# Optimization experiments

Hardware: AMD Instinct MI355X
Metric: run time of the kernel (lower is better)

## Reference

```python
import jax, jax.numpy as jnp
import numpy as np

N, F, H = 100000, 128, 2
DH = F // H  # per-head dim = 64
E = 1600000


def setup_inputs() -> dict:
    key = jax.random.key(0)
    ks = jax.random.split(key, 10)
    s = 0.05
    return {
        "nodes": jax.random.normal(ks[0], (N, F), jnp.float32),
        "edge_index": jax.random.randint(ks[1], (2, E), 0, N, jnp.int64),
        # TransformerConv linear layers (stored as [in, out] so we do x @ W)
        "Wq": jax.random.normal(ks[2], (F, F), jnp.float32) * s,
        "bq": jnp.zeros((F,), jnp.float32),
        "Wk": jax.random.normal(ks[3], (F, F), jnp.float32) * s,
        "bk": jnp.zeros((F,), jnp.float32),
        "Wv": jax.random.normal(ks[4], (F, F), jnp.float32) * s,
        "bv": jnp.zeros((F,), jnp.float32),
        "Wskip": jax.random.normal(ks[5], (F, F), jnp.float32) * s,
        "bskip": jnp.zeros((F,), jnp.float32),
        # gate: Linear(2F, F, bias=False); fuse: Linear(F, F, bias=False)
        "Wgate": jax.random.normal(ks[6], (2 * F, F), jnp.float32) * s,
        "Wfuse": jax.random.normal(ks[7], (F, F), jnp.float32) * s,
    }


def transformer_conv(nodes, src, dst, Wq, bq, Wk, bk, Wv, bv, Wskip, bskip):
    n = nodes.shape[0]
    q = (nodes @ Wq + bq).reshape(n, H, DH)
    k = (nodes @ Wk + bk).reshape(n, H, DH)
    v = (nodes @ Wv + bv).reshape(n, H, DH)
    # per-edge attention logits: [E, H]
    alpha = jnp.einsum("ehd,ehd->eh", q[dst], k[src]) / jnp.sqrt(jnp.float32(DH))
    # segment softmax over incoming edges of each destination node
    amax = jax.ops.segment_max(alpha, dst, num_segments=n)  # [N, H]
    ex = jnp.exp(alpha - amax[dst])
    denom = jax.ops.segment_sum(ex, dst, num_segments=n)  # [N, H]
    w = ex / denom[dst]  # [E, H]
    msg = v[src] * w[:, :, None]  # [E, H, DH]
    agg = jax.ops.segment_sum(msg, dst, num_segments=n).reshape(n, F)
    # root/skip connection (beta=0 -> plain add)
    return agg + nodes @ Wskip + bskip


def reference(nodes, edge_index, Wq, bq, Wk, bk, Wv, bv, Wskip, bskip, Wgate, Wfuse):
    src, dst = edge_index[0], edge_index[1]
    x = transformer_conv(nodes, src, dst, Wq, bq, Wk, bk, Wv, bv, Wskip, bskip)
    h = jnp.concatenate([nodes, x], axis=-1)  # [N, 2F]
    gate = jax.nn.sigmoid(h @ Wgate)  # [N, F]
    fuse = jnp.tanh(x @ Wfuse)  # [N, F]
    return gate * fuse + (1.0 - gate) * nodes
```

## Files before the change

kernel.cpp:

```cpp
#include <hip/hip_runtime.h>
#include <hip/hip_fp8.h>
#include <stdint.h>

#define NN 100000
#define EE 1600000
#define FF 128
#define CAP 60

typedef __attribute__((ext_vector_type(8)))  short bf16x8;
typedef __attribute__((ext_vector_type(8)))  unsigned short u16x8;
typedef __attribute__((ext_vector_type(2)))  float f32x2;
typedef __attribute__((ext_vector_type(16))) float f32x16;

#define NB_BLOCKS    6250
#define PREP_BLOCKS  450
#define CNT0_BLOCKS  98
#define BUILD2_BLOCKS 1563
#define QKVS_BLOCKS  12500
#define F2_BLOCKS    (BUILD2_BLOCKS + QKVS_BLOCKS)

__device__ __forceinline__ float bf2f(unsigned short u) {
    union { unsigned int i; float f; } c; c.i = ((unsigned int)u) << 16; return c.f;
}
__device__ __forceinline__ unsigned short f2bf(float f) {
    union { unsigned int i; float f; } c; c.f = f;
    unsigned int u = c.i;
    return (unsigned short)((u + 0x7FFFu + ((u >> 16) & 1u)) >> 16);
}
__device__ __forceinline__ float fp82f(unsigned int b) {
    __hip_fp8_e4m3 t; t.__x = (__hip_fp8_storage_t)(b & 0xFFu); return (float)t;
}
__device__ __forceinline__ unsigned char f2fp8(float f) {
    __hip_fp8_e4m3 t(f); return (unsigned char)t.__x;
}
template<bool HI>
__device__ __forceinline__ f32x2 cvtpk8(unsigned int w) {
#if __has_builtin(__builtin_amdgcn_cvt_pk_f32_fp8)
    return __builtin_amdgcn_cvt_pk_f32_fp8((int)w, HI);
#else
    f32x2 r;
    r[0] = fp82f(HI ? (w >> 16) : w);
    r[1] = fp82f(HI ? (w >> 24) : (w >> 8));
    return r;
#endif
}
__device__ __forceinline__ bf16x8 pack8(const float* p) {
    float4 f0 = *(const float4*)p;
    float4 f1 = *(const float4*)(p + 4);
    bf16x8 r;
    r[0] = (short)f2bf(f0.x); r[1] = (short)f2bf(f0.y);
    r[2] = (short)f2bf(f0.z); r[3] = (short)f2bf(f0.w);
    r[4] = (short)f2bf(f1.x); r[5] = (short)f2bf(f1.y);
    r[6] = (short)f2bf(f1.z); r[7] = (short)f2bf(f1.w);
    return r;
}

__global__ __launch_bounds__(256) void k_f1(
    const float* __restrict__ nodes, unsigned short* __restrict__ nb,
    const float* __restrict__ Wq, const float* __restrict__ Wk,
    const float* __restrict__ Wv, const float* __restrict__ Ws,
    const float* __restrict__ Wg, const float* __restrict__ Wf,
    const float* __restrict__ bq, const float* __restrict__ bk,
    const float* __restrict__ bv, const float* __restrict__ bs,
    unsigned short* __restrict__ Wp, unsigned short* __restrict__ Wp2,
    float* __restrict__ bias, int* __restrict__ count)
{
    const int bid = blockIdx.x;
    if (bid < NB_BLOCKS) {
        size_t i = ((size_t)bid * 256 + threadIdx.x) * 8;
        *(bf16x8*)(nb + i) = pack8(nodes + i);
    } else if (bid < NB_BLOCKS + PREP_BLOCKS) {
        int idx = (bid - NB_BLOCKS) * 256 + threadIdx.x;
        if (idx < 65536) {
            int j = idx & 7, lane = (idx >> 3) & 63, ks = (idx >> 9) & 7;
            int cf = (idx >> 12) & 3, cg = idx >> 14;
            int c  = cf * 32 + (lane & 31);
            int kk = ks * 16 + (lane >> 5) * 8 + j;
            const float* W = (cg == 0) ? Wq : (cg == 1) ? Wk : (cg == 2) ? Wv : Ws;
            Wp[idx] = f2bf(W[kk * FF + c]);
        } else if (idx < 65536 + 49152) {
            int p = idx - 65536;
            int j = p & 7, lane = (p >> 3) & 63, ks = (p >> 9) & 7;
            int cf = (p >> 12) & 3, mat = p >> 14;
            int c  = cf * 32 + (lane & 31);
            int kk = ks * 16 + (lane >> 5) * 8 + j;
            float v = (mat == 0) ? Wg[kk * FF + c]
                    : (mat == 1) ? Wg[(FF + kk) * FF + c]
                                 : Wf[kk * FF + c];
            Wp2[p] = f2bf(v);
        } else if (idx < 65536 + 49152 + 512) {
            int j = idx - (65536 + 49152);
            float b = (j < 128) ? bq[j] : (j < 256) ? bk[j - 128]
                    : (j < 384) ? bv[j - 256] : bs[j - 384];
            bias[j] = b;
        }
    } else {
        int j = ((bid - NB_BLOCKS - PREP_BLOCKS) * 256 + threadIdx.x) * 4;
        if (j < NN) *(int4*)(count + j) = make_int4(0, 0, 0, 0);
    }
}

__global__ __launch_bounds__(256) void k_f2(
    const int* __restrict__ src, const int* __restrict__ dst,
    int* __restrict__ count, int* __restrict__ srclist,
    const unsigned short* __restrict__ nb, const unsigned short* __restrict__ Wp,
    const float* __restrict__ bias, unsigned short* __restrict__ qb,
    unsigned char* __restrict__ kvb, unsigned short* __restrict__ skb)
{
    const int bid = blockIdx.x;
    if (bid % 9 == 0) {
        const int bb = bid / 9;
        const int e0 = bb * 1024 + threadIdx.x;
        #pragma unroll
        for (int j = 0; j < 4; ++j) {
            const int e = e0 + j * 256;
            if (e < EE) {
                int d = dst[e];
                int s = src[e];
                int r = atomicAdd(&count[d], 1);
                if (r < CAP) __builtin_nontemporal_store(s, &srclist[(size_t)d * CAP + r]);
            }
        }
        return;
    }
    const int q = bid - bid / 9 - 1;
    const int row0 = (q >> 2) * 32;
    const int cg = q & 3;
    const int wave = threadIdx.x >> 6, lane = threadIdx.x & 63;
    const int arow = row0 + (lane & 31);
    const int khalf = lane >> 5;
    const int cf = wave;

    f32x16 acc;
    #pragma unroll
    for (int r = 0; r < 16; ++r) acc[r] = 0.f;

    const unsigned short* ap = nb + (size_t)arow * FF + khalf * 8;
    #pragma unroll
    for (int ks = 0; ks < 8; ++ks) {
        bf16x8 a = *(const bf16x8*)(ap + ks * 16);
        bf16x8 b = *(const bf16x8*)(Wp + (((cg * 4 + cf) * 8 + ks) << 9) + (lane << 3));
        acc = __builtin_amdgcn_mfma_f32_32x32x16_bf16(a, b, acc, 0, 0, 0);
    }

    const int col = cf * 32 + (lane & 31);
    const float bv = bias[cg * 128 + col];
    #pragma unroll
    for (int r = 0; r < 16; ++r) {
        const int rr = row0 + (r & 3) + 8 * (r >> 2) + 4 * (lane >> 5);
        const float fv = acc[r] + bv;
        if (cg == 0)      qb [(size_t)rr * 128 + col] = f2bf(fv);
        else if (cg == 1) kvb[(size_t)rr * 256 + (col >> 2) * 8 + (col & 3)]     = f2fp8(fv);
        else if (cg == 2) kvb[(size_t)rr * 256 + (col >> 2) * 8 + 4 + (col & 3)] = f2fp8(fv);
        else              skb[(size_t)rr * 128 + col] = f2bf(fv);
    }
}

__global__ __launch_bounds__(256, 4) void k_f3(
    const unsigned short* __restrict__ nb, const unsigned short* __restrict__ qb,
    const unsigned char* __restrict__ kvb, const unsigned short* __restrict__ skb,
    const unsigned short* __restrict__ Wp2,
    const int* __restrict__ count, const int* __restrict__ srclist,
    float* __restrict__ out)
{
    __shared__ unsigned short xl[32 * 128];
    const int wave = threadIdx.x >> 6, lane = threadIdx.x & 63;
    const int row0 = blockIdx.x * 32;

    const int es = lane >> 4;
    const int le = lane & 15;

    #pragma unroll 1
    for (int i = 0; i < 8; ++i) {
        const int rl  = wave * 8 + i;
        const int wid = row0 + rl;

        const u16x8 qr = *(const u16x8*)(qb + (size_t)wid * FF + le * 8);
        float qa[8];
        #pragma unroll
        for (int j = 0; j < 8; ++j) qa[j] = bf2f(qr[j]) * 0.125f;

        int deg = __builtin_amdgcn_readfirstlane(count[wid]);
        if (deg > CAP) deg = CAP;
        const size_t base = (size_t)wid * CAP;
        const int sreg = srclist[base + (lane < CAP ? lane : CAP - 1)];

        float denom = 0.f;
        float acc[8];
        #pragma unroll
        for (int j = 0; j < 8; ++j) acc[j] = 0.f;

        const int nit = (deg + 3) >> 2;
        #pragma unroll 2
        for (int it = 0; it < nit; ++it) {
            const int idx  = 4 * it + es;
            const int sidx = idx < deg ? idx : deg - 1;
            const int s    = __shfl(sreg, sidx);
            const uint4 kv = *(const uint4*)(kvb + (size_t)s * 256 + le * 16);
            const f32x2 k01 = cvtpk8<false>(kv.x), k23 = cvtpk8<true>(kv.x);
            const f32x2 k45 = cvtpk8<false>(kv.z), k67 = cvtpk8<true>(kv.z);
            float p = qa[0] * k01[0] + qa[1] * k01[1] + qa[2] * k23[0] + qa[3] * k23[1]
                    + qa[4] * k45[0] + qa[5] * k45[1] + qa[6] * k67[0] + qa[7] * k67[1];
            p += __shfl_xor(p, 1);
            p += __shfl_xor(p, 2);
            p += __shfl_xor(p, 4);
            const float ex = (idx < deg) ? __expf(p) : 0.f;
            denom += ex;
            const f32x2 v01 = cvtpk8<false>(kv.y), v23 = cvtpk8<true>(kv.y);
            const f32x2 v45 = cvtpk8<false>(kv.w), v67 = cvtpk8<true>(kv.w);
            acc[0] = fmaf(ex, v01[0], acc[0]); acc[1] = fmaf(ex, v01[1], acc[1]);
            acc[2] = fmaf(ex, v23[0], acc[2]); acc[3] = fmaf(ex, v23[1], acc[3]);
            acc[4] = fmaf(ex, v45[0], acc[4]); acc[5] = fmaf(ex, v45[1], acc[5]);
            acc[6] = fmaf(ex, v67[0], acc[6]); acc[7] = fmaf(ex, v67[1], acc[7]);
        }
        denom += __shfl_xor(denom, 16);
        denom += __shfl_xor(denom, 32);
        #pragma unroll
        for (int j = 0; j < 8; ++j) {
            acc[j] += __shfl_xor(acc[j], 16);
            acc[j] += __shfl_xor(acc[j], 32);
        }

        if (es == 0) {
            const float inv = (denom > 0.f) ? (1.0f / denom) : 0.f;
            const u16x8 sr = *(const u16x8*)(skb + (size_t)wid * FF + le * 8);
            u16x8 o;
            #pragma unroll
            for (int j = 0; j < 8; ++j) o[j] = f2bf(fmaf(acc[j], inv, bf2f(sr[j])));
            *(u16x8*)&xl[rl * 128 + ((le ^ (rl & 7)) << 3)] = o;
        }
    }
    __syncthreads();

    const int arow = row0 + (lane & 31);
    const int khalf = lane >> 5;
    const int cf = wave;

    f32x16 gacc, facc;
    #pragma unroll
    for (int r = 0; r < 16; ++r) { gacc[r] = 0.f; facc[r] = 0.f; }

    #pragma unroll
    for (int ks = 0; ks < 8; ++ks) {
        bf16x8 an = *(const bf16x8*)(nb + (size_t)arow * FF + ks * 16 + khalf * 8);
        const int g2 = ks * 2 + khalf;
        bf16x8 ax = *(const bf16x8*)&xl[(lane & 31) * 128 + ((g2 ^ ((lane & 31) & 7)) << 3)];
        bf16x8 b0 = *(const bf16x8*)(Wp2 + (((0 * 4 + cf) * 8 + ks) << 9) + (lane << 3));
        bf16x8 b1 = *(const bf16x8*)(Wp2 + (((1 * 4 + cf) * 8 + ks) << 9) + (lane << 3));
        bf16x8 b2 = *(const bf16x8*)(Wp2 + (((2 * 4 + cf) * 8 + ks) << 9) + (lane << 3));
        gacc = __builtin_amdgcn_mfma_f32_32x32x16_bf16(an, b0, gacc, 0, 0, 0);
        gacc = __builtin_amdgcn_mfma_f32_32x32x16_bf16(ax, b1, gacc, 0, 0, 0);
        facc = __builtin_amdgcn_mfma_f32_32x32x16_bf16(ax, b2, facc, 0, 0, 0);
    }

    const int col = cf * 32 + (lane & 31);
    #pragma unroll
    for (int r = 0; r < 16; ++r) {
        const int rr = row0 + (r & 3) + 8 * (r >> 2) + 4 * (lane >> 5);
        const float g  = 1.0f / (1.0f + __expf(-gacc[r]));
        const float e2 = __expf(2.0f * facc[r]);
        const float fv = (e2 - 1.0f) / (e2 + 1.0f);
        const float nv = bf2f(nb[(size_t)rr * FF + col]);
        out[(size_t)rr * FF + col] = g * fv + (1.0f - g) * nv;
    }
}

extern "C" void kernel_launch(void* const* d_in, const int* in_sizes, int n_in,
                              void* d_out, int out_size, void* d_ws, size_t ws_size,
                              hipStream_t stream) {
    const float* nodes = (const float*)d_in[0];
    const int*   ei    = (const int*)d_in[1];
    const int*   esrc  = ei;
    const int*   edst  = ei + EE;
    const float* Wq = (const float*)d_in[2];
    const float* bq = (const float*)d_in[3];
    const float* Wk = (const float*)d_in[4];
    const float* bk = (const float*)d_in[5];
    const float* Wv = (const float*)d_in[6];
    const float* bv = (const float*)d_in[7];
    const float* Ws = (const float*)d_in[8];
    const float* bs = (const float*)d_in[9];
    const float* Wg = (const float*)d_in[10];
    const float* Wf = (const float*)d_in[11];
    float* out = (float*)d_out;

    char* wsb = (char*)d_ws;
    unsigned short* qb   = (unsigned short*)wsb;
    unsigned char*  kvb  = (unsigned char*)(qb + (size_t)NN * 128);
    unsigned short* skb  = (unsigned short*)(kvb + (size_t)NN * 256);
    unsigned short* nb   = skb + (size_t)NN * 128;
    unsigned short* Wp   = nb + (size_t)NN * 128;
    unsigned short* Wp2  = Wp + 65536;
    float* bias  = (float*)(Wp2 + 49152);
    int* count   = (int*)(bias + 512);
    int* srclist = count + NN;

    k_f1<<<NB_BLOCKS + PREP_BLOCKS + CNT0_BLOCKS, 256, 0, stream>>>(
        nodes, nb, Wq, Wk, Wv, Ws, Wg, Wf, bq, bk, bv, bs, Wp, Wp2, bias, count);
    k_f2<<<F2_BLOCKS, 256, 0, stream>>>(
        esrc, edst, count, srclist, nb, Wp, bias, qb, kvb, skb);
    k_f3<<<NN / 32, 256, 0, stream>>>(
        nb, qb, kvb, skb, Wp2, count, srclist, out);
}
```

Baseline: 233.7 us.

## Prefetch next row's metadata and use packed math in attention aggregation loop

In the fused aggregation kernel, the per-row loads (degree count, query, source list, skip row) for the next destination row are issued one iteration ahead, so their latency can overlap with the current row's edge loop. The dot product and value accumulation are rewritten with float2 vectors so the compiler can emit packed FMA instructions. The 1/8 query scale is folded together with log2(e) so that exp2f can stand in for __expf. Edge index loads in the CSR build now use nontemporal loads, and the edge loop unroll goes from 2 to 4. These changes add register pressure, which may affect occupancy under the 256,4 launch bounds.

```diff
diff --git a/kernel.cpp b/kernel.cpp
--- a/kernel.cpp
+++ b/kernel.cpp
@@ -18,6 +18,8 @@
 #define BUILD2_BLOCKS 1563
 #define QKVS_BLOCKS  12500
 #define F2_BLOCKS    (BUILD2_BLOCKS + QKVS_BLOCKS)
+
+#define QSCALE 0.1803368801111244f
 
 __device__ __forceinline__ float bf2f(unsigned short u) {
     union { unsigned int i; float f; } c; c.i = ((unsigned int)u) << 16; return c.f;
@@ -115,8 +117,8 @@
         for (int j = 0; j < 4; ++j) {
             const int e = e0 + j * 256;
             if (e < EE) {
-                int d = dst[e];
-                int s = src[e];
+                int d = __builtin_nontemporal_load(&dst[e]);
+                int s = __builtin_nontemporal_load(&src[e]);
                 int r = atomicAdd(&count[d], 1);
                 if (r < CAP) __builtin_nontemporal_store(s, &srclist[(size_t)d * CAP + r]);
             }
@@ -169,64 +171,81 @@
 
     const int es = lane >> 4;
     const int le = lane & 15;
+    const int slane = lane < CAP ? lane : CAP - 1;
+
+    {
+        const int wid0 = row0 + wave * 8;
+    }
+    int   deg_n  = count[row0 + wave * 8];
+    u16x8 qr_n   = *(const u16x8*)(qb  + (size_t)(row0 + wave * 8) * FF + le * 8);
+    int   sreg_n = srclist[(size_t)(row0 + wave * 8) * CAP + slane];
+    u16x8 sr_n   = *(const u16x8*)(skb + (size_t)(row0 + wave * 8) * FF + le * 8);
 
     #pragma unroll 1
     for (int i = 0; i < 8; ++i) {
         const int rl  = wave * 8 + i;
         const int wid = row0 + rl;
 
-        const u16x8 qr = *(const u16x8*)(qb + (size_t)wid * FF + le * 8);
-        float qa[8];
-        #pragma unroll
-        for (int j = 0; j < 8; ++j) qa[j] = bf2f(qr[j]) * 0.125f;
-
-        int deg = __builtin_amdgcn_readfirstlane(count[wid]);
+        int deg = __builtin_amdgcn_readfirstlane(deg_n);
         if (deg > CAP) deg = CAP;
-        const size_t base = (size_t)wid * CAP;
-        const int sreg = srclist[base + (lane < CAP ? lane : CAP - 1)];
+        const u16x8 qr  = qr_n;
+        const int   sreg = sreg_n;
+        const u16x8 sr  = sr_n;
+
+        if (i < 7) {
+            const int widn = wid + 1;
+            deg_n  = count[widn];
+            qr_n   = *(const u16x8*)(qb  + (size_t)widn * FF + le * 8);
+            sreg_n = srclist[(size_t)widn * CAP + slane];
+            sr_n   = *(const u16x8*)(skb + (size_t)widn * FF + le * 8);
+        }
+
+        f32x2 qa0, qa1, qa2, qa3;
+        qa0[0] = bf2f(qr[0]) * QSCALE; qa0[1] = bf2f(qr[1]) * QSCALE;
+        qa1[0] = bf2f(qr[2]) * QSCALE; qa1[1] = bf2f(qr[3]) * QSCALE;
+        qa2[0] = bf2f(qr[4]) * QSCALE; qa2[1] = bf2f(qr[5]) * QSCALE;
+        qa3[0] = bf2f(qr[6]) * QSCALE; qa3[1] = bf2f(qr[7]) * QSCALE;
 
         float denom = 0.f;
-        float acc[8];
-        #pragma unroll
-        for (int j = 0; j < 8; ++j) acc[j] = 0.f;
+        f32x2 a01 = {0.f, 0.f}, a23 = {0.f, 0.f}, a45 = {0.f, 0.f}, a67 = {0.f, 0.f};
 
         const int nit = (deg + 3) >> 2;
-        #pragma unroll 2
+        #pragma unroll 4
         for (int it = 0; it < nit; ++it) {
             const int idx  = 4 * it + es;
             const int sidx = idx < deg ? idx : deg - 1;
             const int s    = __shfl(sreg, sidx);
             const uint4 kv = *(const uint4*)(kvb + (size_t)s * 256 + le * 16);
-            const f32x2 k01 = cvtpk8<false>(kv.x), k23 = cvtpk8<true>(kv.x);
-            const f32x2 k45 = cvtpk8<false>(kv.z), k67 = cvtpk8<true>(kv.z);
-            float p = qa[0] * k01[0] + qa[1] * k01[1] + qa[2] * k23[0] + qa[3] * k23[1]
-                    + qa[4] * k45[0] + qa[5] * k45[1] + qa[6] * k67[0] + qa[7] * k67[1];
+            f32x2 pp = qa0 * cvtpk8<false>(kv.x);
+            pp += qa1 * cvtpk8<true>(kv.x);
+            pp += qa2 * cvtpk8<false>(kv.z);
+            pp += qa3 * cvtpk8<true>(kv.z);
+            float p = pp[0] + pp[1];
             p += __shfl_xor(p, 1);
             p += __shfl_xor(p, 2);
             p += __shfl_xor(p, 4);
-            const float ex = (idx < deg) ? __expf(p) : 0.f;
+            const float ex = (idx < deg) ? exp2f(p) : 0.f;
             denom += ex;
-            const f32x2 v01 = cvtpk8<false>(kv.y), v23 = cvtpk8<true>(kv.y);
-            const f32x2 v45 = cvtpk8<false>(kv.w), v67 = cvtpk8<true>(kv.w);
-            acc[0] = fmaf(ex, v01[0], acc[0]); acc[1] = fmaf(ex, v01[1], acc[1]);
-            acc[2] = fmaf(ex, v23[0], acc[2]); acc[3] = fmaf(ex, v23[1], acc[3]);
-            acc[4] = fmaf(ex, v45[0], acc[4]); acc[5] = fmaf(ex, v45[1], acc[5]);
-            acc[6] = fmaf(ex, v67[0], acc[6]); acc[7] = fmaf(ex, v67[1], acc[7]);
+            f32x2 exv; exv[0] = ex; exv[1] = ex;
+            a01 += exv * cvtpk8<false>(kv.y);
+            a23 += exv * cvtpk8<true>(kv.y);
+            a45 += exv * cvtpk8<false>(kv.w);
+            a67 += exv * cvtpk8<true>(kv.w);
         }
         denom += __shfl_xor(denom, 16);
         denom += __shfl_xor(denom, 32);
+        float af[8] = {a01[0], a01[1], a23[0], a23[1], a45[0], a45[1], a67[0], a67[1]};
         #pragma unroll
         for (int j = 0; j < 8; ++j) {
-            acc[j] += __shfl_xor(acc[j], 16);
-            acc[j] += __shfl_xor(acc[j], 32);
+            af[j] += __shfl_xor(af[j], 16);
+            af[j] += __shfl_xor(af[j], 32);
         }
 
         if (es == 0) {
             const float inv = (denom > 0.f) ? (1.0f / denom) : 0.f;
-            const u16x8 sr = *(const u16x8*)(skb + (size_t)wid * FF + le * 8);
             u16x8 o;
             #pragma unroll
-            for (int j = 0; j < 8; ++j) o[j] = f2bf(fmaf(acc[j], inv, bf2f(sr[j])));
+            for (int j = 0; j < 8; ++j) o[j] = f2bf(fmaf(af[j], inv, bf2f(sr[j])));
             *(u16x8*)&xl[rl * 128 + ((le ^ (rl & 7)) << 3)] = o;
         }
     }
```

After: 249.3 us. +6.7%, slower.
